# Kernel optimization log

Measured on AMD Instinct MI355X. Metric: run time of the kernel, lower is better.

Reference implementation:

```python
import jax, jax.numpy as jnp
import numpy as np

NEG_SLOPE = 0.2  # PyG GATConv leaky_relu slope


def _gat_conv(x, src, dst, W, a_s, a_d, b, H, D, concat):
    """PyG-style GATConv (eval mode, self-loops already in src/dst).
    x: [N, F_in], W: [F_in, H*D], a_s/a_d: [H, D], b: [H*D] or [D]."""
    N = x.shape[0]
    h = (x @ W).reshape(N, H, D)                      # [N, H, D]
    al_src = (h * a_s).sum(-1)                        # [N, H]
    al_dst = (h * a_d).sum(-1)                        # [N, H]
    e = jax.nn.leaky_relu(al_src[src] + al_dst[dst], NEG_SLOPE)   # [E, H]
    m = jax.ops.segment_max(e, dst, num_segments=N)               # [N, H]
    m = jnp.where(jnp.isfinite(m), m, 0.0)
    ex = jnp.exp(e - m[dst])
    denom = jax.ops.segment_sum(ex, dst, num_segments=N)
    alpha = ex / (denom[dst] + 1e-16)                 # edge softmax per dst node
    out = jax.ops.segment_sum(alpha[:, :, None] * h[src], dst, num_segments=N)  # [N, H, D]
    out = out.reshape(N, H * D) if concat else out.mean(axis=1)
    return out + b


def setup_inputs() -> dict:
    key = jax.random.key(0)
    ks = jax.random.split(key, 14)
    N, E, F_in, H, D, OUT = 50000, 800000, 256, 8, 32, 64
    g = lambda k, shape, fan: (jax.random.normal(k, shape, jnp.float32) / np.float32(np.sqrt(fan)))
    return {
        "x": jax.random.normal(ks[0], (N, F_in), jnp.float32),
        "edge_index": jax.random.randint(ks[1], (2, E), 0, N),
        # conv0: GATConv(256 -> 32, heads=8, concat)
        "W0": g(ks[2], (F_in, H * D), F_in),
        "a_src0": g(ks[3], (H, D), D),
        "a_dst0": g(ks[4], (H, D), D),
        "b0": jnp.zeros((H * D,), jnp.float32),
        # residual0: Linear(256 -> 256)
        "Wr0": g(ks[5], (F_in, H * D), F_in),
        "br0": jnp.zeros((H * D,), jnp.float32),
        # conv1: GATConv(256 -> 64, heads=1, concat=False)
        "W1": g(ks[6], (H * D, OUT), H * D),
        "a_src1": g(ks[7], (1, OUT), OUT),
        "a_dst1": g(ks[8], (1, OUT), OUT),
        "b1": jnp.zeros((OUT,), jnp.float32),
        # residual1: Linear(256 -> 64)
        "Wr1": g(ks[9], (H * D, OUT), H * D),
        "br1": jnp.zeros((OUT,), jnp.float32),
    }


def reference(x, edge_index, W0, a_src0, a_dst0, b0, Wr0, br0, W1, a_src1, a_dst1, b1, Wr1, br1):
    N = x.shape[0]
    loops = jnp.arange(N, dtype=edge_index.dtype)
    src = jnp.concatenate([edge_index[0], loops])   # add self loops
    dst = jnp.concatenate([edge_index[1], loops])
    # layer 0: GATConv + residual + ELU (dropout is identity in eval)
    h = _gat_conv(x, src, dst, W0, a_src0, a_dst0, b0, 8, 32, True)
    h = jax.nn.elu(h + (x @ Wr0 + br0))
    # final layer: heads=1, concat=False, + residual
    out = _gat_conv(h, src, dst, W1, a_src1, a_dst1, b1, 1, 64, False)
    out = out + (h @ Wr1 + br1)
    return jax.nn.log_softmax(out, axis=1)
```

## Files before the change

kernel.cpp:

```cpp
#include <hip/hip_runtime.h>
#include <math.h>

#define NEG_SLOPE 0.2f
#define BSH 7
#define NBLK_PART 256

typedef __attribute__((ext_vector_type(8))) short bf16x8;
typedef __attribute__((ext_vector_type(4))) float f32x4;
typedef __attribute__((ext_vector_type(2))) float f32x2;
typedef __attribute__((ext_vector_type(8))) unsigned short ushort8;
typedef __attribute__((ext_vector_type(4))) unsigned short ushort4v;

__device__ __forceinline__ float b2f(unsigned short u){
  return __uint_as_float(((unsigned)u) << 16);
}
__device__ __forceinline__ unsigned short f2b(float f){
  unsigned u = __float_as_uint(f);
  return (unsigned short)((u + 0x7FFFu + ((u >> 16) & 1u)) >> 16);
}

#if __has_builtin(__builtin_amdgcn_cvt_pk_f32_fp8) && __has_builtin(__builtin_amdgcn_cvt_pk_fp8_f32)
#define HW_FP8 1
#else
#define HW_FP8 0
#endif

#if !HW_FP8
__device__ __forceinline__ unsigned enc8_one(float f){
  unsigned bits = __float_as_uint(f);
  unsigned s = bits >> 31;
  unsigned e = (bits >> 23) & 255;
  unsigned mant = bits & 0x7FFFFF;
  if(e < 121){
    float af = fabsf(f);
    int m = (int)(af * 512.f + 0.5f);
    if(m > 7) m = 7;
    return (s << 7) | (unsigned)m;
  }
  unsigned lsb = (mant >> 20) & 1;
  mant += 0x7FFFF + lsb;
  if(mant >> 23){ e += 1; mant = 0; }
  unsigned m3 = mant >> 20;
  unsigned e8 = e - 120;
  if(e8 > 15 || (e8 == 15 && m3 == 7)) return (s << 7) | 0x7E;
  return (s << 7) | (e8 << 3) | m3;
}
#endif

template<bool HI>
__device__ __forceinline__ unsigned enc8_pair(float a, float b, unsigned old){
#if HW_FP8
  return __builtin_amdgcn_cvt_pk_fp8_f32(a, b, old, HI);
#else
  unsigned p = enc8_one(a) | (enc8_one(b) << 8);
  return HI ? ((old & 0x0000FFFFu) | (p << 16)) : ((old & 0xFFFF0000u) | p);
#endif
}

__device__ __forceinline__ unsigned char enc8b(float v){
  return (unsigned char)(enc8_pair<false>(v, v, 0u) & 0xFFu);
}

__device__ __forceinline__ void dec8x4v(unsigned q, f32x2& lo, f32x2& hi){
#if HW_FP8
  lo = __builtin_amdgcn_cvt_pk_f32_fp8(q, false);
  hi = __builtin_amdgcn_cvt_pk_f32_fp8(q, true);
#else
  auto dec1 = [](unsigned b)->float{
    unsigned s = (b >> 7) & 1, e = (b >> 3) & 15, m = b & 7;
    float v = (e == 0) ? (float)m * 0.001953125f
                       : __uint_as_float(((e + 120) << 23) | (m << 20));
    return s ? -v : v;
  };
  lo[0] = dec1(q & 255); lo[1] = dec1((q >> 8) & 255);
  hi[0] = dec1((q >> 16) & 255); hi[1] = dec1(q >> 24);
#endif
}

extern "C" __global__ void k_part1(const int* __restrict__ dsts, int E, int N,
                                   int NBUCK, int* __restrict__ bcnt,
                                   int* __restrict__ blockbase){
  __shared__ int hist[512];
  int blk = blockIdx.x, tid = threadIdx.x;
  for(int b = tid; b < NBUCK; b += 256) hist[b] = 0;
  __syncthreads();
  int ET = E + N;
  int chunk = (ET + NBLK_PART - 1)/NBLK_PART;
  int s0 = blk*chunk, s1 = s0+chunk < ET ? s0+chunk : ET;
  for(int e = s0+tid; e < s1; e += 256){
    int d = (e < E) ? dsts[e] : e - E;
    atomicAdd(&hist[d >> BSH], 1);
  }
  __syncthreads();
  for(int b = tid; b < NBUCK; b += 256)
    blockbase[(size_t)blk*NBUCK + b] = atomicAdd(&bcnt[b], hist[b]);
}

extern "C" __global__ void k_bscan(const int* __restrict__ bcnt, int* __restrict__ boffs,
                                   int* __restrict__ offs_last, int NBUCK, int ET){
  __shared__ int sc[512], orig[512];
  int t = threadIdx.x;
  int v = (t < NBUCK) ? bcnt[t] : 0;
  sc[t] = v; orig[t] = v;
  __syncthreads();
  for(int st=1; st<512; st<<=1){
    int u = (t >= st) ? sc[t-st] : 0;
    __syncthreads();
    sc[t] += u;
    __syncthreads();
  }
  if(t < NBUCK) boffs[t] = sc[t] - orig[t];
  if(t == 0){ boffs[NBUCK] = ET; *offs_last = ET; }
}

extern "C" __global__ void k_part2(const int* __restrict__ srcs, const int* __restrict__ dsts,
                                   int E, int N, int NBUCK,
                                   const int* __restrict__ boffs, const int* __restrict__ blockbase,
                                   uint2* __restrict__ pairs){
  __shared__ int cur[512];
  int blk = blockIdx.x, tid = threadIdx.x;
  for(int b = tid; b < NBUCK; b += 256)
    cur[b] = boffs[b] + blockbase[(size_t)blk*NBUCK + b];
  __syncthreads();
  int ET = E + N;
  int chunk = (ET + NBLK_PART - 1)/NBLK_PART;
  int s0 = blk*chunk, s1 = s0+chunk < ET ? s0+chunk : ET;
  for(int e = s0+tid; e < s1; e += 256){
    int s, d;
    if(e < E){ s = srcs[e]; d = dsts[e]; } else { s = d = e - E; }
    int pos = atomicAdd(&cur[d >> BSH], 1);
    uint2 pr; pr.x = (unsigned)d; pr.y = (unsigned)s;
    pairs[pos] = pr;
  }
}

extern "C" __global__ void k_bcsr(const uint2* __restrict__ pairs, const int* __restrict__ boffs,
                                  int N, int* __restrict__ offs, int* __restrict__ csr){
  __shared__ int hist[128], sc[128], lcur[128];
  int b = blockIdx.x, tid = threadIdx.x;
  int node0 = b << BSH;
  int base = boffs[b], endp = boffs[b+1];
  if(tid < 128) hist[tid] = 0;
  __syncthreads();
  for(int i = base + tid; i < endp; i += 256)
    atomicAdd(&hist[pairs[i].x & 127], 1);
  __syncthreads();
  if(tid < 128) sc[tid] = hist[tid];
  __syncthreads();
  for(int st=1; st<128; st<<=1){
    int u = (tid < 128 && tid >= st) ? sc[tid-st] : 0;
    __syncthreads();
    if(tid < 128) sc[tid] += u;
    __syncthreads();
  }
  if(tid < 128){
    int ex = sc[tid] - hist[tid];
    lcur[tid] = ex;
    int n = node0 + tid;
    if(n < N) offs[n] = base + ex;
  }
  __syncthreads();
  for(int i = base + tid; i < endp; i += 256){
    uint2 pr = pairs[i];
    int pos = atomicAdd(&lcur[pr.x & 127], 1);
    csr[base + pos] = (int)pr.y;
  }
}

extern "C" __global__ void k_wt2(const float* __restrict__ W0, const float* __restrict__ Wr0,
                                 const float* __restrict__ W1, const float* __restrict__ Wr1,
                                 unsigned short* __restrict__ WT0, unsigned short* __restrict__ WT1){
  int idx = blockIdx.x*256 + threadIdx.x;
  const int tot0 = 512*256;
  if(idx < tot0){
    int n = idx >> 8, k = idx & 255;
    const float* W = (n < 256) ? W0 : Wr0;
    int c = (n < 256) ? n : n - 256;
    WT0[idx] = f2b(W[(size_t)k*256 + c]);
  } else {
    idx -= tot0;
    if(idx >= 128*256) return;
    int n = idx >> 8, k = idx & 255;
    const float* W = (n < 64) ? W1 : Wr1;
    int c = (n < 64) ? n : n - 64;
    WT1[idx] = f2b(W[(size_t)k*64 + c]);
  }
}

__launch_bounds__(256)
extern "C" __global__ void k_mgemm(const unsigned short* __restrict__ A,
                                   const float* __restrict__ Afp,
                                   const unsigned short* __restrict__ WT,
                                   unsigned short* __restrict__ C, int ldc, int M,
                                   int MB, int NCB,
                                   unsigned char* __restrict__ qout, int qcols){
  int id = blockIdx.x;
  int row_blk, col_blk;
  if(NCB == 4){
    int group = id >> 5;
    int r8 = id & 7;
    col_blk = (id >> 3) & 3;
    row_blk = group*8 + r8;
  } else {
    row_blk = id; col_blk = 0;
  }
  if(row_blk >= MB) return;

  __shared__ unsigned short As[128*64];
  __shared__ unsigned short Bs[128*64];
  int t = threadIdx.x;
  int lane = t & 63, wid = t >> 6;
  int wr = wid >> 1, wc = wid & 1;
  int row0 = row_blk*128, col0 = col_blk*128;
  f32x4 acc[4][4] = {};

  float4 v0s[4], v1s[4];
  const float* abase[4];
  if(Afp){
    #pragma unroll
    for(int i=0; i<4; i++){
      int t2 = i*256 + t;
      int r = t2 >> 3;
      int dslot = (t2 & 7) ^ (r & 7);
      int gr = row0 + r; if(gr >= M) gr = M - 1;
      abase[i] = Afp + (size_t)gr*256 + dslot*8;
      v0s[i] = *(const float4*)(abase[i]);
      v1s[i] = *(const float4*)(abase[i] + 4);
    }
  }

  for(int k0 = 0; k0 < 256; k0 += 64){
    if(Afp){
      #pragma unroll
      for(int i=0; i<4; i++){
        ushort8 o;
        o[0]=f2b(v0s[i].x); o[1]=f2b(v0s[i].y); o[2]=f2b(v0s[i].z); o[3]=f2b(v0s[i].w);
        o[4]=f2b(v1s[i].x); o[5]=f2b(v1s[i].y); o[6]=f2b(v1s[i].z); o[7]=f2b(v1s[i].w);
        *(ushort8*)(As + i*2048 + wid*512 + lane*8) = o;
      }
    } else {
      #pragma unroll
      for(int i=0; i<4; i++){
        int t2 = i*256 + t;
        int r = t2 >> 3;
        int dslot = (t2 & 7) ^ (r & 7);
        int gr = row0 + r; if(gr >= M) gr = M - 1;
        const unsigned short* ga = A + (size_t)gr*256 + k0 + dslot*8;
        __builtin_amdgcn_global_load_lds((const __attribute__((address_space(1))) unsigned*)ga,
            (__attribute__((address_space(3))) unsigned*)(As + i*2048 + wid*512), 16, 0, 0);
      }
    }
    #pragma unroll
    for(int i=0; i<4; i++){
      int t2 = i*256 + t;
      int r = t2 >> 3;
      int dslot = (t2 & 7) ^ (r & 7);
      const unsigned short* gb = WT + (size_t)(col0 + r)*256 + k0 + dslot*8;
      __builtin_amdgcn_global_load_lds((const __attribute__((address_space(1))) unsigned*)gb,
          (__attribute__((address_space(3))) unsigned*)(Bs + i*2048 + wid*512), 16, 0, 0);
    }
    __syncthreads();
    if(Afp && k0 < 192){
      #pragma unroll
      for(int i=0; i<4; i++){
        v0s[i] = *(const float4*)(abase[i] + k0 + 64);
        v1s[i] = *(const float4*)(abase[i] + k0 + 68);
      }
    }
    #pragma unroll
    for(int kc=0; kc<2; kc++){
      bf16x8 a[4], b[4];
      int kb = kc*4 + (lane >> 4);
      #pragma unroll
      for(int f=0; f<4; f++){
        int ar = wr*64 + f*16 + (lane & 15);
        a[f] = *(const bf16x8*)&As[ar*64 + ((kb ^ (ar & 7))*8)];
        int br = wc*64 + f*16 + (lane & 15);
        b[f] = *(const bf16x8*)&Bs[br*64 + ((kb ^ (br & 7))*8)];
      }
      #pragma unroll
      for(int fm=0; fm<4; fm++)
        #pragma unroll
        for(int fn=0; fn<4; fn++)
          acc[fm][fn] = __builtin_amdgcn_mfma_f32_16x16x32_bf16(a[fm], b[fn], acc[fm][fn], 0, 0, 0);
    }
    __syncthreads();
  }

  int rb = row0 + wr*64 + ((lane >> 4) << 2);
  int cb = col0 + wc*64 + (lane & 15);
  #pragma unroll
  for(int fm=0; fm<4; fm++){
    #pragma unroll
    for(int r=0; r<4; r++){
      int row = rb + fm*16 + r;
      if(row < M){
        #pragma unroll
        for(int fn=0; fn<4; fn++)
          C[(size_t)row*ldc + cb + fn*16] = f2b(acc[fm][fn][r]);
        if(qout){
          #pragma unroll
          for(int fn=0; fn<4; fn++){
            int col = cb + fn*16;
            if(col < qcols) qout[(size_t)row*qcols + col] = enc8b(acc[fm][fn][r]);
          }
        }
      }
    }
  }
}

extern "C" __global__ void k_al0(const unsigned short* __restrict__ buf0b, const float* __restrict__ as0,
                                 const float* __restrict__ ad0, float* als0, float* ald0, int N){
  int i = blockIdx.x*blockDim.x + threadIdx.x;
  if(i >= N*8) return;
  int n = i >> 3, h = i & 7;
  const uint4* hp = (const uint4*)(buf0b + (size_t)n*512 + h*32);
  const float* av = as0 + h*32;
  const float* dv = ad0 + h*32;
  float s = 0.f, d = 0.f;
  #pragma unroll
  for(int q=0; q<4; q++){
    uint4 u = hp[q];
    unsigned w[4] = {u.x, u.y, u.z, u.w};
    #pragma unroll
    for(int j=0; j<4; j++){
      float lo = __uint_as_float(w[j] << 16);
      float hi = __uint_as_float(w[j] & 0xFFFF0000u);
      int c = q*8 + j*2;
      s += lo*av[c] + hi*av[c+1];
      d += lo*dv[c] + hi*dv[c+1];
    }
  }
  als0[i] = s; ald0[i] = d;
}

__launch_bounds__(256)
extern "C" __global__ void k_gather0(const unsigned short* __restrict__ buf0b,
                                     const unsigned char* __restrict__ h0q,
                                     const float* __restrict__ als0, const float* __restrict__ ald0,
                                     const int* __restrict__ offs, const int* __restrict__ csr,
                                     const float* __restrict__ b0, const float* __restrict__ br0,
                                     unsigned short* __restrict__ h1b, int N){
  int n = blockIdx.x*4 + (threadIdx.x >> 6);
  if(n >= N) return;
  int lane = threadIdx.x & 63;
  int hh = lane & 7;
  int es = lane >> 3;
  int h  = es;
  int c  = lane*4;
  float ald_h = ald0[n*8 + hh];
  int beg = offs[n], end = offs[n+1];

  f32x2 A01 = {0.f, 0.f}, A23 = {0.f, 0.f};
  float den = 0.f;

  for(int chunk = beg; chunk < end; chunk += 8){
    int m = end - chunk; if(m > 8) m = 8;
    bool e_ok = es < m;
    int s = e_ok ? csr[chunk + es] : 0;
    float p = 0.f;
    if(e_ok){
      float v = als0[s*8 + hh] + ald_h;
      v = v > 0.f ? v : NEG_SLOPE*v;
      p = expf(v);
    }
    den += p;
    int sj[8]; float pj[8];
    #pragma unroll
    for(int j=0; j<8; j++){
      sj[j] = __shfl(s, j*8);
      pj[j] = __shfl(p, j*8 + h);
    }
    unsigned q[8];
    #pragma unroll
    for(int j=0; j<8; j++)
      q[j] = *(const unsigned*)(h0q + (size_t)sj[j]*256 + c);
    #pragma unroll
    for(int j=0; j<8; j++){
      f32x2 lo, hi, pv;
      dec8x4v(q[j], lo, hi);
      pv[0] = pj[j]; pv[1] = pj[j];
      A01 += pv*lo; A23 += pv*hi;
    }
  }

  den += __shfl_xor(den, 8);
  den += __shfl_xor(den, 16);
  den += __shfl_xor(den, 32);
  float rden = 1.f/(den + 1e-16f);
  rden = __shfl(rden, h);

  float a0 = A01[0]*rden, a1 = A01[1]*rden, a2 = A23[0]*rden, a3 = A23[1]*rden;

  float4 bb = *(const float4*)(b0 + c);
  float4 rb = *(const float4*)(br0 + c);
  uint2 ru = *(const uint2*)(buf0b + (size_t)n*512 + 256 + c);
  float o0 = a0 + bb.x + __uint_as_float(ru.x << 16)         + rb.x;
  float o1 = a1 + bb.y + __uint_as_float(ru.x & 0xFFFF0000u) + rb.y;
  float o2 = a2 + bb.z + __uint_as_float(ru.y << 16)         + rb.z;
  float o3 = a3 + bb.w + __uint_as_float(ru.y & 0xFFFF0000u) + rb.w;
  ushort4v o;
  o[0] = f2b(o0 > 0.f ? o0 : expf(o0) - 1.f);
  o[1] = f2b(o1 > 0.f ? o1 : expf(o1) - 1.f);
  o[2] = f2b(o2 > 0.f ? o2 : expf(o2) - 1.f);
  o[3] = f2b(o3 > 0.f ? o3 : expf(o3) - 1.f);
  *(ushort4v*)(h1b + (size_t)n*256 + c) = o;
}

extern "C" __global__ void k_al1(const unsigned short* __restrict__ buf1b, const float* __restrict__ as1,
                                 const float* __restrict__ ad1, float* als1, float* ald1, int N){
  int n = blockIdx.x*4 + (threadIdx.x >> 6);
  if(n >= N) return;
  int lane = threadIdx.x & 63;
  float g = b2f(buf1b[(size_t)n*128 + lane]);
  float s = g*as1[lane], d = g*ad1[lane];
  #pragma unroll
  for(int o=32; o>0; o>>=1){ s += __shfl_xor(s,o); d += __shfl_xor(d,o); }
  if(lane == 0){ als1[n] = s; ald1[n] = d; }
}

__launch_bounds__(256)
extern "C" __global__ void k_gather1(const unsigned short* __restrict__ buf1b,
                                     const unsigned char* __restrict__ g1q,
                                     const float* __restrict__ als1, const float* __restrict__ ald1,
                                     const int* __restrict__ offs, const int* __restrict__ csr,
                                     const float* __restrict__ b1, const float* __restrict__ br1,
                                     float* __restrict__ out, int N){
  int n = blockIdx.x*4 + (threadIdx.x >> 6);
  if(n >= N) return;
  int lane = threadIdx.x & 63;
  int ch4 = lane & 15;
  int es  = lane >> 4;
  int c   = ch4*4;
  int beg = offs[n], end = offs[n+1];
  float ald_n = ald1[n];

  f32x2 A01 = {0.f, 0.f}, A23 = {0.f, 0.f};
  float den = 0.f;

  for(int chunk = beg; chunk < end; chunk += 64){
    int m = end - chunk; if(m > 64) m = 64;
    int s = (lane < m) ? csr[chunk + lane] : 0;
    float p = 0.f;
    if(lane < m){
      float v = als1[s] + ald_n;
      v = v > 0.f ? v : NEG_SLOPE*v;
      p = expf(v);
    }
    den += p;
    for(int base = 0; base < m; base += 16){
      int sv[4]; float pv[4];
      #pragma unroll
      for(int i=0; i<4; i++){
        int j = base + 4*i + es;
        int jj = j & 63;
        sv[i] = __shfl(s, jj);
        pv[i] = __shfl(p, jj);
      }
      unsigned qv[4];
      #pragma unroll
      for(int i=0; i<4; i++)
        qv[i] = *(const unsigned*)(g1q + (size_t)sv[i]*64 + c);
      #pragma unroll
      for(int i=0; i<4; i++){
        f32x2 lo, hi, pp;
        dec8x4v(qv[i], lo, hi);
        pp[0] = pv[i]; pp[1] = pv[i];
        A01 += pp*lo; A23 += pp*hi;
      }
    }
  }

  A01[0] += __shfl_xor(A01[0], 16); A01[1] += __shfl_xor(A01[1], 16);
  A23[0] += __shfl_xor(A23[0], 16); A23[1] += __shfl_xor(A23[1], 16);
  A01[0] += __shfl_xor(A01[0], 32); A01[1] += __shfl_xor(A01[1], 32);
  A23[0] += __shfl_xor(A23[0], 32); A23[1] += __shfl_xor(A23[1], 32);
  #pragma unroll
  for(int o=32; o>0; o>>=1) den += __shfl_xor(den, o);
  float rden = 1.f/(den + 1e-16f);

  float4 bb = *(const float4*)(b1 + c);
  float4 rb = *(const float4*)(br1 + c);
  uint2 ru = *(const uint2*)(buf1b + (size_t)n*128 + 64 + c);
  float v0 = A01[0]*rden + bb.x + __uint_as_float(ru.x << 16)         + rb.x;
  float v1 = A01[1]*rden + bb.y + __uint_as_float(ru.x & 0xFFFF0000u) + rb.y;
  float v2 = A23[0]*rden + bb.z + __uint_as_float(ru.y << 16)         + rb.z;
  float v3 = A23[1]*rden + bb.w + __uint_as_float(ru.y & 0xFFFF0000u) + rb.w;

  float mx = fmaxf(fmaxf(v0, v1), fmaxf(v2, v3));
  #pragma unroll
  for(int o=1; o<16; o<<=1) mx = fmaxf(mx, __shfl_xor(mx, o));
  float sm = expf(v0-mx) + expf(v1-mx) + expf(v2-mx) + expf(v3-mx);
  #pragma unroll
  for(int o=1; o<16; o<<=1) sm += __shfl_xor(sm, o);
  float l = mx + logf(sm);
  if(es == 0){
    float4 ov; ov.x = v0-l; ov.y = v1-l; ov.z = v2-l; ov.w = v3-l;
    *(float4*)(out + (size_t)n*64 + c) = ov;
  }
}

extern "C" void kernel_launch(void* const* d_in, const int* in_sizes, int n_in,
                              void* d_out, int out_size, void* d_ws, size_t ws_size,
                              hipStream_t stream){
  const float* x   = (const float*)d_in[0];
  const int*   ei  = (const int*)  d_in[1];
  const float* W0  = (const float*)d_in[2];
  const float* as0 = (const float*)d_in[3];
  const float* ad0 = (const float*)d_in[4];
  const float* b0  = (const float*)d_in[5];
  const float* Wr0 = (const float*)d_in[6];
  const float* br0 = (const float*)d_in[7];
  const float* W1  = (const float*)d_in[8];
  const float* as1 = (const float*)d_in[9];
  const float* ad1 = (const float*)d_in[10];
  const float* b1  = (const float*)d_in[11];
  const float* Wr1 = (const float*)d_in[12];
  const float* br1 = (const float*)d_in[13];
  int N = in_sizes[0] / 256;
  int E = in_sizes[1] / 2;
  const int* srcs = ei;
  const int* dsts = ei + E;
  float* out = (float*)d_out;

  int ET = E + N;
  int NBUCK = (N + 127) >> BSH;

  unsigned short* buf0b = (unsigned short*)d_ws;
  unsigned short* xb    = buf0b + (size_t)N*512;
  unsigned short* h1b   = xb    + (size_t)N*256;
  unsigned short* buf1b = h1b   + (size_t)N*256;
  unsigned short* WT0   = buf1b + (size_t)N*128;
  unsigned short* WT1   = WT0   + 512*256;
  float*    als0 = (float*)(WT1 + 128*256);
  float*    ald0 = als0 + (size_t)N*8;
  float*    als1 = ald0 + (size_t)N*8;
  float*    ald1 = als1 + N;
  int*      offs = (int*)(ald1 + N);
  int*      bcnt = offs + N + 1;
  int*      boffs = bcnt + NBUCK;
  int*      blockbase = boffs + NBUCK + 1;
  int*      csr  = blockbase + (size_t)NBLK_PART*NBUCK;
  uint2*    pairs = (uint2*)(csr + ET);
  pairs = (uint2*)(((uintptr_t)pairs + 7) & ~(uintptr_t)7);
  unsigned char* g1q = (unsigned char*)(pairs + ET);
  unsigned char* h0q = (unsigned char*)xb;

  hipMemsetAsync(bcnt, 0, (size_t)NBUCK*sizeof(int), stream);
  hipLaunchKernelGGL(k_part1, dim3(NBLK_PART), dim3(256), 0, stream, dsts, E, N, NBUCK, bcnt, blockbase);
  hipLaunchKernelGGL(k_bscan, dim3(1), dim3(512), 0, stream, bcnt, boffs, offs + N, NBUCK, ET);
  hipLaunchKernelGGL(k_part2, dim3(NBLK_PART), dim3(256), 0, stream, srcs, dsts, E, N, NBUCK, boffs, blockbase, pairs);
  hipLaunchKernelGGL(k_bcsr, dim3(NBUCK), dim3(256), 0, stream, pairs, boffs, N, offs, csr);

  hipLaunchKernelGGL(k_wt2, dim3((512*256+128*256+255)/256), dim3(256), 0, stream, W0, Wr0, W1, Wr1, WT0, WT1);

  int MB = (N + 127) / 128;
  int g0 = ((MB + 7) / 8) * 32;
  hipLaunchKernelGGL(k_mgemm, dim3(g0), dim3(256), 0, stream,
                     (const unsigned short*)nullptr, x, WT0, buf0b, 512, N, MB, 4, h0q, 256);
  hipLaunchKernelGGL(k_al0, dim3((N*8+255)/256), dim3(256), 0, stream, buf0b, as0, ad0, als0, ald0, N);
  hipLaunchKernelGGL(k_gather0, dim3((N+3)/4), dim3(256), 0, stream, buf0b, h0q, als0, ald0, offs, csr, b0, br0, h1b, N);

  hipLaunchKernelGGL(k_mgemm, dim3(MB), dim3(256), 0, stream,
                     h1b, (const float*)nullptr, WT1, buf1b, 128, N, MB, 1, g1q, 64);
  hipLaunchKernelGGL(k_al1, dim3((N+3)/4), dim3(256), 0, stream, buf1b, as1, ad1, als1, ald1, N);
  hipLaunchKernelGGL(k_gather1, dim3((N+3)/4), dim3(256), 0, stream, buf1b, g1q, als1, ald1, offs, csr, b1, br1, out, N);
}
```

Measured before the change: 197.6 us.

## Fuse attention-logit computation into GEMM epilogue via LDS-staged coalesced stores

The GEMM epilogue now stages the accumulator tile through shared memory and writes vectorized rows. In layer 0 it computes the per-head source and destination attention dot products there and emits only the fp8 features and the residual half. This removes the separate k_al0 kernel and avoids writing and rereading the bf16 copy of h0. It also replaces scattered per-element bf16/fp8 stores with coalesced 16-byte and 8-byte stores. In exchange it adds an extra LDS pass and barrier, and the attention logits are now computed from bf16-rounded values.

Result: faster. 181.4 us (-8.2%).

```diff
diff --git a/kernel.cpp b/kernel.cpp
--- a/kernel.cpp
+++ b/kernel.cpp
@@ -55,10 +55,6 @@
   unsigned p = enc8_one(a) | (enc8_one(b) << 8);
   return HI ? ((old & 0x0000FFFFu) | (p << 16)) : ((old & 0xFFFF0000u) | p);
 #endif
-}
-
-__device__ __forceinline__ unsigned char enc8b(float v){
-  return (unsigned char)(enc8_pair<false>(v, v, 0u) & 0xFFu);
 }
 
 __device__ __forceinline__ void dec8x4v(unsigned q, f32x2& lo, f32x2& hi){
@@ -191,9 +187,12 @@
 extern "C" __global__ void k_mgemm(const unsigned short* __restrict__ A,
                                    const float* __restrict__ Afp,
                                    const unsigned short* __restrict__ WT,
-                                   unsigned short* __restrict__ C, int ldc, int M,
-                                   int MB, int NCB,
-                                   unsigned char* __restrict__ qout, int qcols){
+                                   unsigned short* __restrict__ C, int M,
+                                   int MB, int NCB, int mode,
+                                   unsigned char* __restrict__ qout,
+                                   unsigned short* __restrict__ rout,
+                                   const float* __restrict__ as0v, const float* __restrict__ ad0v,
+                                   float* __restrict__ alsout, float* __restrict__ aldout){
   int id = blockIdx.x;
   int row_blk, col_blk;
   if(NCB == 4){
@@ -206,8 +205,9 @@
   }
   if(row_blk >= MB) return;
 
-  __shared__ unsigned short As[128*64];
-  __shared__ unsigned short Bs[128*64];
+  __shared__ unsigned short SH[128*128];
+  unsigned short* As = SH;
+  unsigned short* Bs = SH + 128*64;
   int t = threadIdx.x;
   int lane = t & 63, wid = t >> 6;
   int wr = wid >> 1, wc = wid & 1;
@@ -287,56 +287,81 @@
     __syncthreads();
   }
 
-  int rb = row0 + wr*64 + ((lane >> 4) << 2);
-  int cb = col0 + wc*64 + (lane & 15);
   #pragma unroll
   for(int fm=0; fm<4; fm++){
-    #pragma unroll
-    for(int r=0; r<4; r++){
-      int row = rb + fm*16 + r;
-      if(row < M){
-        #pragma unroll
-        for(int fn=0; fn<4; fn++)
-          C[(size_t)row*ldc + cb + fn*16] = f2b(acc[fm][fn][r]);
-        if(qout){
-          #pragma unroll
-          for(int fn=0; fn<4; fn++){
-            int col = cb + fn*16;
-            if(col < qcols) qout[(size_t)row*qcols + col] = enc8b(acc[fm][fn][r]);
+    int rl = wr*64 + fm*16 + ((lane>>4)<<2);
+    #pragma unroll
+    for(int r=0; r<4; r++)
+      #pragma unroll
+      for(int fn=0; fn<4; fn++)
+        SH[(rl+r)*128 + wc*64 + (lane&15) + fn*16] = f2b(acc[fm][fn][r]);
+  }
+  __syncthreads();
+
+  int cg = t & 15;
+  if(mode == 0){
+    bool attn = col_blk < 2;
+    int colbase = col0 + cg*8;
+    float4 as_lo, as_hi, ad_lo, ad_hi;
+    if(attn){
+      as_lo = *(const float4*)(as0v + colbase);
+      as_hi = *(const float4*)(as0v + colbase + 4);
+      ad_lo = *(const float4*)(ad0v + colbase);
+      ad_hi = *(const float4*)(ad0v + colbase + 4);
+    }
+    #pragma unroll
+    for(int it=0; it<8; it++){
+      int rl = it*16 + (t>>4);
+      int row = row0 + rl;
+      ushort8 vr = *(ushort8*)&SH[rl*128 + cg*8];
+      if(attn){
+        float f0=b2f(vr[0]),f1=b2f(vr[1]),f2=b2f(vr[2]),f3=b2f(vr[3]);
+        float f4=b2f(vr[4]),f5=b2f(vr[5]),f6=b2f(vr[6]),f7=b2f(vr[7]);
+        float sd = f0*as_lo.x+f1*as_lo.y+f2*as_lo.z+f3*as_lo.w
+                 + f4*as_hi.x+f5*as_hi.y+f6*as_hi.z+f7*as_hi.w;
+        float dd = f0*ad_lo.x+f1*ad_lo.y+f2*ad_lo.z+f3*ad_lo.w
+                 + f4*ad_hi.x+f5*ad_hi.y+f6*ad_hi.z+f7*ad_hi.w;
+        sd += __shfl_xor(sd,1); sd += __shfl_xor(sd,2);
+        dd += __shfl_xor(dd,1); dd += __shfl_xor(dd,2);
+        uint2 q;
+        q.x = enc8_pair<false>(f0,f1,0u); q.x = enc8_pair<true>(f2,f3,q.x);
+        q.y = enc8_pair<false>(f4,f5,0u); q.y = enc8_pair<true>(f6,f7,q.y);
+        if(row < M){
+          *(uint2*)(qout + (size_t)row*256 + colbase) = q;
+          if((lane&3)==0){
+            int head = colbase >> 5;
+            alsout[row*8 + head] = sd;
+            aldout[row*8 + head] = dd;
           }
         }
-      }
-    }
-  }
-}
-
-extern "C" __global__ void k_al0(const unsigned short* __restrict__ buf0b, const float* __restrict__ as0,
-                                 const float* __restrict__ ad0, float* als0, float* ald0, int N){
-  int i = blockIdx.x*blockDim.x + threadIdx.x;
-  if(i >= N*8) return;
-  int n = i >> 3, h = i & 7;
-  const uint4* hp = (const uint4*)(buf0b + (size_t)n*512 + h*32);
-  const float* av = as0 + h*32;
-  const float* dv = ad0 + h*32;
-  float s = 0.f, d = 0.f;
-  #pragma unroll
-  for(int q=0; q<4; q++){
-    uint4 u = hp[q];
-    unsigned w[4] = {u.x, u.y, u.z, u.w};
-    #pragma unroll
-    for(int j=0; j<4; j++){
-      float lo = __uint_as_float(w[j] << 16);
-      float hi = __uint_as_float(w[j] & 0xFFFF0000u);
-      int c = q*8 + j*2;
-      s += lo*av[c] + hi*av[c+1];
-      d += lo*dv[c] + hi*dv[c+1];
-    }
-  }
-  als0[i] = s; ald0[i] = d;
+      } else {
+        if(row < M)
+          *(ushort8*)(rout + (size_t)row*256 + (colbase - 256)) = vr;
+      }
+    }
+  } else {
+    #pragma unroll
+    for(int it=0; it<8; it++){
+      int rl = it*16 + (t>>4);
+      int row = row0 + rl;
+      ushort8 vr = *(ushort8*)&SH[rl*128 + cg*8];
+      if(row < M){
+        *(ushort8*)(C + (size_t)row*128 + cg*8) = vr;
+        if(cg < 8){
+          float f0=b2f(vr[0]),f1=b2f(vr[1]),f2=b2f(vr[2]),f3=b2f(vr[3]);
+          float f4=b2f(vr[4]),f5=b2f(vr[5]),f6=b2f(vr[6]),f7=b2f(vr[7]);
+          uint2 q;
+          q.x = enc8_pair<false>(f0,f1,0u); q.x = enc8_pair<true>(f2,f3,q.x);
+          q.y = enc8_pair<false>(f4,f5,0u); q.y = enc8_pair<true>(f6,f7,q.y);
+          *(uint2*)(qout + (size_t)row*64 + cg*8) = q;
+        }
+      }
+    }
+  }
 }
 
 __launch_bounds__(256)
-extern "C" __global__ void k_gather0(const unsigned short* __restrict__ buf0b,
+extern "C" __global__ void k_gather0(const unsigned short* __restrict__ r0b,
                                      const unsigned char* __restrict__ h0q,
                                      const float* __restrict__ als0, const float* __restrict__ ald0,
                                      const int* __restrict__ offs, const int* __restrict__ csr,
@@ -395,7 +420,7 @@
 
   float4 bb = *(const float4*)(b0 + c);
   float4 rb = *(const float4*)(br0 + c);
-  uint2 ru = *(const uint2*)(buf0b + (size_t)n*512 + 256 + c);
+  uint2 ru = *(const uint2*)(r0b + (size_t)n*256 + c);
   float o0 = a0 + bb.x + __uint_as_float(ru.x << 16)         + rb.x;
   float o1 = a1 + bb.y + __uint_as_float(ru.x & 0xFFFF0000u) + rb.y;
   float o2 = a2 + bb.z + __uint_as_float(ru.y << 16)         + rb.z;
@@ -527,10 +552,10 @@
   int ET = E + N;
   int NBUCK = (N + 127) >> BSH;
 
-  unsigned short* buf0b = (unsigned short*)d_ws;
-  unsigned short* xb    = buf0b + (size_t)N*512;
-  unsigned short* h1b   = xb    + (size_t)N*256;
-  unsigned short* buf1b = h1b   + (size_t)N*256;
+  unsigned short* r0b   = (unsigned short*)d_ws;
+  unsigned char*  h0q   = (unsigned char*)(r0b + (size_t)N*256);
+  unsigned short* h1b   = (unsigned short*)(h0q + (size_t)N*256);
+  unsigned short* buf1b = h1b + (size_t)N*256;
   unsigned short* WT0   = buf1b + (size_t)N*128;
   unsigned short* WT1   = WT0   + 512*256;
   float*    als0 = (float*)(WT1 + 128*256);
@@ -545,7 +570,6 @@
   uint2*    pairs = (uint2*)(csr + ET);
   pairs = (uint2*)(((uintptr_t)pairs + 7) & ~(uintptr_t)7);
   unsigned char* g1q = (unsigned char*)(pairs + ET);
-  unsigned char* h0q = (unsigned char*)xb;
 
   hipMemsetAsync(bcnt, 0, (size_t)NBUCK*sizeof(int), stream);
   hipLaunchKernelGGL(k_part1, dim3(NBLK_PART), dim3(256), 0, stream, dsts, E, N, NBUCK, bcnt, blockbase);
@@ -558,12 +582,17 @@
   int MB = (N + 127) / 128;
   int g0 = ((MB + 7) / 8) * 32;
   hipLaunchKernelGGL(k_mgemm, dim3(g0), dim3(256), 0, stream,
-                     (const unsigned short*)nullptr, x, WT0, buf0b, 512, N, MB, 4, h0q, 256);
-  hipLaunchKernelGGL(k_al0, dim3((N*8+255)/256), dim3(256), 0, stream, buf0b, as0, ad0, als0, ald0, N);
-  hipLaunchKernelGGL(k_gather0, dim3((N+3)/4), dim3(256), 0, stream, buf0b, h0q, als0, ald0, offs, csr, b0, br0, h1b, N);
+                     (const unsigned short*)nullptr, x, WT0,
+                     (unsigned short*)nullptr, N, MB, 4, 0,
+                     h0q, r0b, as0, ad0, als0, ald0);
+  hipLaunchKernelGGL(k_gather0, dim3((N+3)/4), dim3(256), 0, stream, r0b, h0q, als0, ald0, offs, csr, b0, br0, h1b, N);
 
   hipLaunchKernelGGL(k_mgemm, dim3(MB), dim3(256), 0, stream,
-                     h1b, (const float*)nullptr, WT1, buf1b, 128, N, MB, 1, g1q, 64);
+                     h1b, (const float*)nullptr, WT1,
+                     buf1b, N, MB, 1, 1,
+                     g1q, (unsigned short*)nullptr,
+                     (const float*)nullptr, (const float*)nullptr,
+                     (float*)nullptr, (float*)nullptr);
   hipLaunchKernelGGL(k_al1, dim3((N+3)/4), dim3(256), 0, stream, buf1b, as1, ad1, als1, ald1, N);
   hipLaunchKernelGGL(k_gather1, dim3((N+3)/4), dim3(256), 0, stream, buf1b, g1q, als1, ald1, offs, csr, b1, br1, out, N);
 }
```
